# Performance work log

Hardware: AMD Instinct MI355X
Metric: run time of the kernel (lower is better)

## Reference

```python
import jax, jax.numpy as jnp
import numpy as np

D_MODEL, D_STATE, D_CONV, EXPAND, MLP_EXPAND = 1024, 16, 4, 2, 2
D_INNER = EXPAND * D_MODEL          # 2048
DT_RANK = D_MODEL // 16             # 64
B, L = 2, 1024


def setup_inputs() -> dict:
    key = jax.random.key(0)
    ks = jax.random.split(key, 16)
    s = 0.02
    inp = {
        "x": jax.random.normal(ks[0], (B, L, D_MODEL), jnp.float32),
        "ln1_w": jnp.ones((D_MODEL,), jnp.float32),
        "ln1_b": jnp.zeros((D_MODEL,), jnp.float32),
        "in_proj_w": jax.random.normal(ks[1], (2 * D_INNER, D_MODEL), jnp.float32) * s,
        "conv_w": jax.random.normal(ks[2], (D_INNER, 1, D_CONV), jnp.float32) * s,
        "conv_b": jnp.zeros((D_INNER,), jnp.float32),
        "x_proj_w": jax.random.normal(ks[3], (DT_RANK + 2 * D_STATE, D_INNER), jnp.float32) * s,
        "dt_proj_w": jax.random.normal(ks[4], (D_INNER, DT_RANK), jnp.float32) * s,
        "dt_proj_b": jax.random.uniform(ks[5], (D_INNER,), jnp.float32, -4.0, -2.0),
        "A_log": jnp.tile(jnp.log(jnp.arange(1, D_STATE + 1, dtype=jnp.float32))[None, :], (D_INNER, 1)),
        "D": jnp.ones((D_INNER,), jnp.float32),
        "out_proj_w": jax.random.normal(ks[6], (D_MODEL, D_INNER), jnp.float32) * s,
        "ln2_w": jnp.ones((D_MODEL,), jnp.float32),
        "ln2_b": jnp.zeros((D_MODEL,), jnp.float32),
        "mlp_w1": jax.random.normal(ks[7], (MLP_EXPAND * D_MODEL, D_MODEL), jnp.float32) * s,
        "mlp_b1": jnp.zeros((MLP_EXPAND * D_MODEL,), jnp.float32),
        "mlp_w2": jax.random.normal(ks[8], (D_MODEL, MLP_EXPAND * D_MODEL), jnp.float32) * s,
        "mlp_b2": jnp.zeros((D_MODEL,), jnp.float32),
    }
    return inp


def _layernorm(x, w, b, eps=1e-5):
    mu = jnp.mean(x, -1, keepdims=True)
    var = jnp.var(x, -1, keepdims=True)
    return (x - mu) * jax.lax.rsqrt(var + eps) * w + b


def _mamba(x, in_proj_w, conv_w, conv_b, x_proj_w, dt_proj_w, dt_proj_b, A_log, D, out_proj_w):
    # x: (B, L, d_model)
    xz = jnp.einsum('bld,ed->ble', x, in_proj_w)          # (B, L, 2*d_inner)
    u, z = jnp.split(xz, 2, axis=-1)                      # each (B, L, d_inner)
    # depthwise causal conv over time
    u_c = jnp.transpose(u, (0, 2, 1))                     # (B, d_inner, L)
    u_c = jax.lax.conv_general_dilated(
        u_c, conv_w, window_strides=(1,), padding=[(D_CONV - 1, 0)],
        dimension_numbers=('NCH', 'OIH', 'NCH'), feature_group_count=D_INNER)
    u = jax.nn.silu(jnp.transpose(u_c, (0, 2, 1)) + conv_b)  # (B, L, d_inner)

    dbc = jnp.einsum('bld,ed->ble', u, x_proj_w)          # (B, L, dt_rank+2*d_state)
    dt, Bm, Cm = jnp.split(dbc, [DT_RANK, DT_RANK + D_STATE], axis=-1)
    delta = jax.nn.softplus(jnp.einsum('blr,dr->bld', dt, dt_proj_w) + dt_proj_b)  # (B, L, d_inner)

    A = -jnp.exp(A_log)                                   # (d_inner, d_state)
    deltaA = jnp.exp(delta[..., None] * A)                # (B, L, d_inner, d_state)
    deltaBu = delta[..., None] * Bm[:, :, None, :] * u[..., None]

    def step(h, inp):
        dA, dBu, Ct = inp
        h = dA * h + dBu                                  # (B, d_inner, d_state)
        y = jnp.einsum('bdn,bn->bd', h, Ct)
        return h, y

    h0 = jnp.zeros((x.shape[0], D_INNER, D_STATE), x.dtype)
    xs = (jnp.moveaxis(deltaA, 1, 0), jnp.moveaxis(deltaBu, 1, 0), jnp.moveaxis(Cm, 1, 0))
    _, ys = jax.lax.scan(step, h0, xs)                    # (L, B, d_inner)
    y = jnp.moveaxis(ys, 0, 1) + u * D                    # (B, L, d_inner)
    y = y * jax.nn.silu(z)
    return jnp.einsum('ble,de->bld', y, out_proj_w)


def reference(x, ln1_w, ln1_b, in_proj_w, conv_w, conv_b, x_proj_w, dt_proj_w, dt_proj_b,
              A_log, D, out_proj_w, ln2_w, ln2_b, mlp_w1, mlp_b1, mlp_w2, mlp_b2):
    h = x + _mamba(_layernorm(x, ln1_w, ln1_b), in_proj_w, conv_w, conv_b,
                   x_proj_w, dt_proj_w, dt_proj_b, A_log, D, out_proj_w)
    y = _layernorm(h, ln2_w, ln2_b)
    y = jax.nn.gelu(jnp.einsum('bld,ed->ble', y, mlp_w1) + mlp_b1, approximate=False)
    y = jnp.einsum('ble,de->bld', y, mlp_w2) + mlp_b2
    return h + y
```

## Files before the change

kernel.cpp:

```cpp
#include <hip/hip_runtime.h>
#include <hip/hip_bf16.h>
#include <math.h>

typedef __hip_bfloat16 bf16;
typedef __attribute__((ext_vector_type(8))) short bf16x8;
typedef __attribute__((ext_vector_type(4))) float f32x4;

__device__ __forceinline__ float b2f(bf16 x) { return __bfloat162float(x); }
__device__ __forceinline__ float us2f(unsigned short u) {
    return __uint_as_float(((unsigned int)u) << 16);
}
__device__ __forceinline__ unsigned short f2us(float f) {
    bf16 t = __float2bfloat16(f);
    return *reinterpret_cast<unsigned short*>(&t);
}
__device__ __forceinline__ float scrub(float v) {
    return (v == v && fabsf(v) < 3.0e38f) ? v : 0.f;
}
__device__ __forceinline__ float to_float(float x) { return x; }
__device__ __forceinline__ float to_float(bf16 x) { return __bfloat162float(x); }
__device__ __forceinline__ void store_out(float* p, float v) { *p = v; }
__device__ __forceinline__ void store_out(bf16* p, float v) { *p = __float2bfloat16(v); }

__device__ __forceinline__ void cp16(const void* g, void* l) {
    __builtin_amdgcn_global_load_lds(
        (const __attribute__((address_space(1))) unsigned int*)g,
        (__attribute__((address_space(3))) unsigned int*)l, 16, 0, 0);
}

struct Ptrs { const void* p[18]; };

__constant__ __device__ const long TOFF[19] = {
    0,         2097152,  2098176,  2099200,  6293504,  6301696,  6303744,
    6500352,   6631424,  6633472,  6666240,  6668288,  8765440,  8766464,
    8767488,   10864640, 10866688, 12963840, 12964864};

__global__ __launch_bounds__(256) void convert_kernel(
    Ptrs ptrs, unsigned short* __restrict__ dst)
{
    const long g = (long)blockIdx.x * 256 + threadIdx.x;
    if (g >= 1620608) return;
    const long e0 = g * 8;
    int t = 0;
    #pragma unroll
    for (int i = 1; i < 18; ++i) t += (e0 >= TOFF[i]) ? 1 : 0;
    const long local = e0 - TOFF[t];
    const float4* ps = (const float4*)((const float*)ptrs.p[t] + local);
    const float4 a = ps[0], b = ps[1];
    ushort4 o0, o1;
    o0.x = f2us(a.x); o0.y = f2us(a.y); o0.z = f2us(a.z); o0.w = f2us(a.w);
    o1.x = f2us(b.x); o1.y = f2us(b.y); o1.z = f2us(b.z); o1.w = f2us(b.w);
    *(ushort4*)(dst + e0)     = o0;
    *(ushort4*)(dst + e0 + 4) = o1;
}

template <typename TIN>
__global__ __launch_bounds__(256) void ln_kernel(
    const TIN* __restrict__ in, const bf16* __restrict__ gw,
    const bf16* __restrict__ gb, bf16* __restrict__ out)
{
    const int row = blockIdx.x;
    const int tid = threadIdx.x;
    float v[4];
    if constexpr (sizeof(TIN) == 2) {
        ushort4 raw = ((const ushort4*)((const unsigned short*)in + (long)row * 1024))[tid];
        v[0] = us2f(raw.x); v[1] = us2f(raw.y); v[2] = us2f(raw.z); v[3] = us2f(raw.w);
    } else {
        float4 raw = ((const float4*)((const float*)in + (long)row * 1024))[tid];
        v[0] = raw.x; v[1] = raw.y; v[2] = raw.z; v[3] = raw.w;
    }
    float s  = v[0] + v[1] + v[2] + v[3];
    float s2 = v[0]*v[0] + v[1]*v[1] + v[2]*v[2] + v[3]*v[3];
    #pragma unroll
    for (int o = 32; o > 0; o >>= 1) {
        s  += __shfl_xor(s, o);
        s2 += __shfl_xor(s2, o);
    }
    __shared__ float red[8];
    if ((tid & 63) == 0) { red[tid >> 6] = s; red[4 + (tid >> 6)] = s2; }
    __syncthreads();
    s  = red[0] + red[1] + red[2] + red[3];
    s2 = red[4] + red[5] + red[6] + red[7];
    const float mu  = s * (1.f / 1024.f);
    const float var = fmaxf(s2 * (1.f / 1024.f) - mu * mu, 0.f);
    const float rs  = rsqrtf(var + 1e-5f);
    const int c0 = tid * 4;
    ushort4 o;
    o.x = f2us((v[0] - mu) * rs * b2f(gw[c0 + 0]) + b2f(gb[c0 + 0]));
    o.y = f2us((v[1] - mu) * rs * b2f(gw[c0 + 1]) + b2f(gb[c0 + 1]));
    o.z = f2us((v[2] - mu) * rs * b2f(gw[c0 + 2]) + b2f(gb[c0 + 2]));
    o.w = f2us((v[3] - mu) * rs * b2f(gw[c0 + 3]) + b2f(gb[c0 + 3]));
    ((ushort4*)((unsigned short*)out + (long)row * 1024))[tid] = o;
}

template <int BM, int BN, int ACT, bool NG, typename TOUT, typename TRES>
__global__ __launch_bounds__(256) void gemm_as(
    const bf16* __restrict__ A, int lda,
    const bf16* __restrict__ Bw, int ldb,
    TOUT* __restrict__ C, int ldc,
    const bf16* __restrict__ bias,
    const TRES* __restrict__ res,
    int M, int N, int K)
{
    constexpr int AI = BM / 32;
    constexpr int BJ = BN / 32;
    __shared__ __align__(16) short As[BM * 64];
    __shared__ __align__(16) short Bs[BN * 64];
    const int tid  = threadIdx.x;
    const int lane = tid & 63;
    const int wv   = tid >> 6;
    const int m0 = blockIdx.y * BM;
    const int n0 = blockIdx.x * BN;
    const int wm = (wv >> 1) * (BM / 2);
    const int wn = (wv & 1) * (BN / 2);
    const int lr = lane & 15;
    const int lq = lane >> 4;
    const int grow = lane >> 3;
    const int gcol = (lane & 7) * 8;

    if (NG) {
        const int z0 = (N - n0) * 64;
        uint4 z; z.x = z.y = z.z = z.w = 0;
        for (int s = z0 + tid * 8; s < BN * 64; s += 2048)
            *(uint4*)&Bs[s] = z;
    }

    f32x4 acc[AI][BJ] = {};

    for (int k0 = 0; k0 < K; k0 += 64) {
        #pragma unroll
        for (int g = 0; g < BM / 32; ++g) {
            const int gg = g * 4 + wv;
            cp16(A + (long)(m0 + gg * 8 + grow) * lda + k0 + gcol, &As[gg * 512]);
        }
        #pragma unroll
        for (int g = 0; g < BN / 32; ++g) {
            const int gg = g * 4 + wv;
            if (!NG || n0 + gg * 8 < N)
                cp16(Bw + (long)(n0 + gg * 8 + grow) * ldb + k0 + gcol, &Bs[gg * 512]);
        }
        __syncthreads();

        #pragma unroll
        for (int kk = 0; kk < 2; ++kk) {
            bf16x8 af[AI], bfr[BJ];
            #pragma unroll
            for (int i = 0; i < AI; ++i)
                af[i] = *(const bf16x8*)&As[(wm + i * 16 + lr) * 64 + kk * 32 + lq * 8];
            #pragma unroll
            for (int j = 0; j < BJ; ++j)
                bfr[j] = *(const bf16x8*)&Bs[(wn + j * 16 + lr) * 64 + kk * 32 + lq * 8];
            #pragma unroll
            for (int i = 0; i < AI; ++i)
                #pragma unroll
                for (int j = 0; j < BJ; ++j)
                    acc[i][j] = __builtin_amdgcn_mfma_f32_16x16x32_bf16(
                        af[i], bfr[j], acc[i][j], 0, 0, 0);
        }
        __syncthreads();
    }

    #pragma unroll
    for (int j = 0; j < BJ; ++j) {
        const int col = n0 + wn + j * 16 + lr;
        if (col >= N) continue;
        const float bv = bias ? b2f(bias[col]) : 0.f;
        #pragma unroll
        for (int i = 0; i < AI; ++i) {
            const int r0 = m0 + wm + i * 16 + lq * 4;
            #pragma unroll
            for (int r = 0; r < 4; ++r) {
                const long row = r0 + r;
                float v = acc[i][j][r] + bv;
                if (ACT == 1) v = 0.5f * v * (1.f + erff(v * 0.70710678118f));
                if (ACT == 2) v = (v > 20.f) ? v : log1pf(__expf(v));
                if (res) v += to_float(res[row * (long)ldc + col]);
                store_out(&C[row * (long)ldc + col], scrub(v));
            }
        }
    }
}

__global__ __launch_bounds__(256) void conv_silu_kernel(
    const bf16* __restrict__ xz, const bf16* __restrict__ cw,
    const bf16* __restrict__ cb, bf16* __restrict__ uc)
{
    const int gid = blockIdx.x * 256 + threadIdx.x;
    const int d   = gid & 2047;
    const int row = gid >> 11;
    const int t   = row & 1023;
    float acc = b2f(cb[d]);
    #pragma unroll
    for (int j = 0; j < 4; ++j) {
        const int tt = t - 3 + j;
        if (tt >= 0)
            acc += b2f(cw[d * 4 + j]) * b2f(xz[(long)(row - 3 + j) * 4096 + d]);
    }
    const float sg = 1.f / (1.f + __expf(-acc));
    uc[gid] = __float2bfloat16(acc * sg);
}

__global__ __launch_bounds__(256) void scan_kernel(
    const bf16* __restrict__ delta,
    const bf16* __restrict__ uc,
    const bf16* __restrict__ dbc,
    const bf16* __restrict__ xz,
    const float* __restrict__ A_log,
    const float* __restrict__ Dp,
    bf16* __restrict__ y)
{
    const int b   = blockIdx.y;
    const int d0  = blockIdx.x * 16;
    const int tid = threadIdx.x;
    const int n   = tid & 15;
    const int dl  = tid >> 4;
    const int d   = d0 + dl;

    __shared__ float2 sDU[64][16];
    __shared__ float2 sBC[64][16];
    __shared__ float  sZ [64][16];
    __shared__ float  sP [64][16][20];

    const float An = -expf(A_log[d * 16 + n]);
    const float Dd = Dp[d];
    float h = 0.f;
    const long rowbase = (long)b * 1024;

    const int dl3 = tid & 15;
    const int t3  = tid >> 4;

    float rDT[4], rUV[4], rB[4], rC[4], rZ[4];
    auto load_chunk = [&](int t0c) {
        #pragma unroll
        for (int k = 0; k < 4; ++k) {
            const int i  = k * 256 + tid;
            const int tt = i >> 4, dd = i & 15;
            const long r = rowbase + t0c + tt;
            rDT[k] = b2f(delta[r * 2048 + d0 + dd]);
            rUV[k] = b2f(uc   [r * 2048 + d0 + dd]);
            rB[k]  = b2f(dbc  [r * 96 + 64 + dd]);
            rC[k]  = b2f(dbc  [r * 96 + 80 + dd]);
            rZ[k]  = b2f(xz   [r * 4096 + 2048 + d0 + dd]);
        }
    };
    auto store_chunk = [&]() {
        #pragma unroll
        for (int k = 0; k < 4; ++k) {
            const int i  = k * 256 + tid;
            const int tt = i >> 4, dd = i & 15;
            sDU[tt][dd] = float2{rDT[k], rUV[k]};
            sBC[tt][dd] = float2{rB[k], rC[k]};
            const float zz = rZ[k];
            sZ[tt][dd] = zz / (1.f + __expf(-zz));
        }
    };

    load_chunk(0);
    for (int t0 = 0; t0 < 1024; t0 += 64) {
        store_chunk();
        __syncthreads();
        if (t0 + 64 < 1024) load_chunk(t0 + 64);

        {
            float2 dua[8], bca[8], dub[8], bcb[8];
            #pragma unroll
            for (int t = 0; t < 8; ++t) { dua[t] = sDU[t][dl]; bca[t] = sBC[t][n]; }
            #pragma unroll
            for (int tb = 0; tb < 64; tb += 8) {
                if (tb < 56) {
                    #pragma unroll
                    for (int t = 0; t < 8; ++t) {
                        dub[t] = sDU[tb + 8 + t][dl];
                        bcb[t] = sBC[tb + 8 + t][n];
                    }
                }
                #pragma unroll
                for (int t = 0; t < 8; ++t) {
                    const float a = __expf(dua[t].x * An);
                    h = a * h + (dua[t].x * dua[t].y) * bca[t].x;
                    float p = h * bca[t].y;
                    if (n == 0) p += dua[t].y * Dd;
                    sP[tb + t][dl][n] = p;
                }
                #pragma unroll
                for (int t = 0; t < 8; ++t) { dua[t] = dub[t]; bca[t] = bcb[t]; }
            }
        }
        __syncthreads();

        #pragma unroll
        for (int k = 0; k < 4; ++k) {
            const int t = t3 + k * 16;
            const float4* pp = (const float4*)&sP[t][dl3][0];
            const float4 p0 = pp[0], p1 = pp[1], p2 = pp[2], p3 = pp[3];
            const float s = ((p0.x + p0.y) + (p0.z + p0.w))
                          + ((p1.x + p1.y) + (p1.z + p1.w))
                          + ((p2.x + p2.y) + (p2.z + p2.w))
                          + ((p3.x + p3.y) + (p3.z + p3.w));
            const float yv = s * sZ[t][dl3];
            y[(rowbase + t0 + t) * 2048 + d0 + dl3] = __float2bfloat16(yv);
        }
        __syncthreads();
    }
}

extern "C" void kernel_launch(void* const* d_in, const int* in_sizes, int n_in,
                              void* d_out, int out_size, void* d_ws, size_t ws_size,
                              hipStream_t stream)
{
    char* ws = (char*)d_ws;
    const size_t MiB = 1048576;

    bf16*  xn  = (bf16*)(ws);
    bf16*  xz  = (bf16*)(ws +  4 * MiB);
    bf16*  uc  = (bf16*)(ws + 20 * MiB);
    bf16*  dbc = (bf16*)(ws + 28 * MiB);
    bf16*  dlb = (bf16*)(ws + 28 * MiB + 524288);
    bf16*  yb  = dlb;
    float* hb  = (float*)(ws);
    bf16*  hn  = (bf16*)(ws +  8 * MiB);
    bf16*  gb  = (bf16*)(ws + 12 * MiB);
    unsigned short* cvt = (unsigned short*)(ws + 37 * MiB);

    const float* xf     = (const float*)d_in[0];
    const float* A_logf = (const float*)d_in[9];
    const float* Dpf    = (const float*)d_in[10];

    const bf16* ln1_w      = (const bf16*)(cvt + 2097152);
    const bf16* ln1_b      = (const bf16*)(cvt + 2098176);
    const bf16* in_proj_w  = (const bf16*)(cvt + 2099200);
    const bf16* conv_w     = (const bf16*)(cvt + 6293504);
    const bf16* conv_b     = (const bf16*)(cvt + 6301696);
    const bf16* x_proj_w   = (const bf16*)(cvt + 6303744);
    const bf16* dt_proj_w  = (const bf16*)(cvt + 6500352);
    const bf16* dt_proj_b  = (const bf16*)(cvt + 6631424);
    const bf16* out_proj_w = (const bf16*)(cvt + 6668288);
    const bf16* ln2_w      = (const bf16*)(cvt + 8765440);
    const bf16* ln2_b      = (const bf16*)(cvt + 8766464);
    const bf16* mlp_w1     = (const bf16*)(cvt + 8767488);
    const bf16* mlp_b1     = (const bf16*)(cvt + 10864640);
    const bf16* mlp_w2     = (const bf16*)(cvt + 10866688);
    const bf16* mlp_b2     = (const bf16*)(cvt + 12963840);

    Ptrs ptrs;
    for (int i = 0; i < 18; ++i) ptrs.p[i] = d_in[i];
    convert_kernel<<<6332, 256, 0, stream>>>(ptrs, cvt);

    ln_kernel<float><<<2048, 256, 0, stream>>>(xf, ln1_w, ln1_b, xn);
    gemm_as<128, 128, 0, false, bf16, bf16><<<dim3(32, 16), 256, 0, stream>>>(
        xn, 1024, in_proj_w, 1024, xz, 4096, nullptr, (const bf16*)nullptr, 2048, 4096, 1024);
    conv_silu_kernel<<<16384, 256, 0, stream>>>(xz, conv_w, conv_b, uc);
    gemm_as<64, 64, 0, true, bf16, bf16><<<dim3(2, 32), 256, 0, stream>>>(
        uc, 2048, x_proj_w, 2048, dbc, 96, nullptr, (const bf16*)nullptr, 2048, 96, 2048);
    gemm_as<64, 64, 2, false, bf16, bf16><<<dim3(32, 32), 256, 0, stream>>>(
        dbc, 96, dt_proj_w, 64, dlb, 2048, dt_proj_b, (const bf16*)nullptr, 2048, 2048, 64);
    scan_kernel<<<dim3(128, 2), 256, 0, stream>>>(dlb, uc, dbc, xz, A_logf, Dpf, yb);
    gemm_as<64, 64, 0, false, float, float><<<dim3(16, 32), 256, 0, stream>>>(
        yb, 2048, out_proj_w, 2048, hb, 1024, nullptr, xf, 2048, 1024, 2048);
    ln_kernel<float><<<2048, 256, 0, stream>>>(hb, ln2_w, ln2_b, hn);
    gemm_as<64, 64, 1, false, bf16, bf16><<<dim3(32, 32), 256, 0, stream>>>(
        hn, 1024, mlp_w1, 1024, gb, 2048, mlp_b1, (const bf16*)nullptr, 2048, 2048, 1024);
    gemm_as<64, 64, 0, false, float, float><<<dim3(16, 32), 256, 0, stream>>>(
        gb, 2048, mlp_w2, 2048, (float*)d_out, 1024, mlp_b2, hb, 2048, 1024, 2048);
}
```

Baseline: 362.8 us.

## Split selective scan into chunked local scan, carry combine, and fix-up passes

Replaces the single sequential scan over 1024 timesteps (256 blocks) with a three-phase chunked scan. The sequence is split into 8 segments of 128 steps, each scanned locally from a zero state (2048 blocks), and the cumulative delta sums are stored in bf16. A small combine kernel then propagates the carried states across segments, and a fix-up kernel adds the C·exp(A·P)·h_in correction to each output. SiLU(z) is moved into the conv kernel, which now writes u and silu(z) interleaved. The goal is more parallelism on the latency-bound scan, at the cost of extra passes, more memory traffic, and bf16 rounding of the cumulative delta inside the exponent.

```diff
diff --git a/kernel.cpp b/kernel.cpp
--- a/kernel.cpp
+++ b/kernel.cpp
@@ -183,7 +183,7 @@
 
 __global__ __launch_bounds__(256) void conv_silu_kernel(
     const bf16* __restrict__ xz, const bf16* __restrict__ cw,
-    const bf16* __restrict__ cb, bf16* __restrict__ uc)
+    const bf16* __restrict__ cb, bf16* __restrict__ ucz)
 {
     const int gid = blockIdx.x * 256 + threadIdx.x;
     const int d   = gid & 2047;
@@ -196,111 +196,186 @@
         if (tt >= 0)
             acc += b2f(cw[d * 4 + j]) * b2f(xz[(long)(row - 3 + j) * 4096 + d]);
     }
-    const float sg = 1.f / (1.f + __expf(-acc));
-    uc[gid] = __float2bfloat16(acc * sg);
-}
-
-__global__ __launch_bounds__(256) void scan_kernel(
+    ucz[(long)row * 4096 + d] = __float2bfloat16(acc / (1.f + __expf(-acc)));
+    const float zz = b2f(xz[(long)row * 4096 + 2048 + d]);
+    ucz[(long)row * 4096 + 2048 + d] = __float2bfloat16(zz / (1.f + __expf(-zz)));
+}
+
+__global__ __launch_bounds__(256) void scan_local_kernel(
     const bf16* __restrict__ delta,
-    const bf16* __restrict__ uc,
+    const bf16* __restrict__ ucz,
     const bf16* __restrict__ dbc,
-    const bf16* __restrict__ xz,
     const float* __restrict__ A_log,
     const float* __restrict__ Dp,
-    bf16* __restrict__ y)
-{
+    bf16* __restrict__ y_local,
+    bf16* __restrict__ Pbuf,
+    float* __restrict__ h_out)
+{
+    const int d0  = blockIdx.x * 16;
     const int b   = blockIdx.y;
-    const int d0  = blockIdx.x * 16;
+    const int sg  = blockIdx.z;
     const int tid = threadIdx.x;
     const int n   = tid & 15;
     const int dl  = tid >> 4;
     const int d   = d0 + dl;
 
-    __shared__ float2 sDU[64][16];
-    __shared__ float2 sBC[64][16];
-    __shared__ float  sZ [64][16];
-    __shared__ float  sP [64][16][20];
+    __shared__ float2         sDU[32][16];
+    __shared__ float2         sBC[32][16];
+    __shared__ float          sZ [32][16];
+    __shared__ unsigned short sPc[32][16];
+    __shared__ unsigned short sY [32][16];
+    __shared__ float          sP [32][16][20];
 
     const float An = -expf(A_log[d * 16 + n]);
     const float Dd = Dp[d];
-    float h = 0.f;
-    const long rowbase = (long)b * 1024;
-
-    const int dl3 = tid & 15;
-    const int t3  = tid >> 4;
-
-    float rDT[4], rUV[4], rB[4], rC[4], rZ[4];
+    float h = 0.f, Pc = 0.f;
+    const long rowbase = (long)b * 1024 + sg * 128;
+
+    const int wv  = tid >> 6;
+    const int pdl = 4 * wv + ((tid & 63) >> 4);
+    const int ptq = tid & 15;
+
+    float rDT[2], rUV[2], rB[2], rC[2], rZ[2];
     auto load_chunk = [&](int t0c) {
         #pragma unroll
-        for (int k = 0; k < 4; ++k) {
+        for (int k = 0; k < 2; ++k) {
             const int i  = k * 256 + tid;
             const int tt = i >> 4, dd = i & 15;
             const long r = rowbase + t0c + tt;
             rDT[k] = b2f(delta[r * 2048 + d0 + dd]);
-            rUV[k] = b2f(uc   [r * 2048 + d0 + dd]);
+            rUV[k] = b2f(ucz  [r * 4096 + d0 + dd]);
             rB[k]  = b2f(dbc  [r * 96 + 64 + dd]);
             rC[k]  = b2f(dbc  [r * 96 + 80 + dd]);
-            rZ[k]  = b2f(xz   [r * 4096 + 2048 + d0 + dd]);
+            rZ[k]  = b2f(ucz  [r * 4096 + 2048 + d0 + dd]);
         }
     };
     auto store_chunk = [&]() {
         #pragma unroll
-        for (int k = 0; k < 4; ++k) {
+        for (int k = 0; k < 2; ++k) {
             const int i  = k * 256 + tid;
             const int tt = i >> 4, dd = i & 15;
             sDU[tt][dd] = float2{rDT[k], rUV[k]};
             sBC[tt][dd] = float2{rB[k], rC[k]};
-            const float zz = rZ[k];
-            sZ[tt][dd] = zz / (1.f + __expf(-zz));
+            sZ[tt][dd]  = rZ[k];
         }
     };
 
     load_chunk(0);
-    for (int t0 = 0; t0 < 1024; t0 += 64) {
+    for (int t0 = 0; t0 < 128; t0 += 32) {
         store_chunk();
         __syncthreads();
-        if (t0 + 64 < 1024) load_chunk(t0 + 64);
-
-        {
-            float2 dua[8], bca[8], dub[8], bcb[8];
-            #pragma unroll
-            for (int t = 0; t < 8; ++t) { dua[t] = sDU[t][dl]; bca[t] = sBC[t][n]; }
-            #pragma unroll
-            for (int tb = 0; tb < 64; tb += 8) {
-                if (tb < 56) {
-                    #pragma unroll
-                    for (int t = 0; t < 8; ++t) {
-                        dub[t] = sDU[tb + 8 + t][dl];
-                        bcb[t] = sBC[tb + 8 + t][n];
-                    }
-                }
-                #pragma unroll
-                for (int t = 0; t < 8; ++t) {
-                    const float a = __expf(dua[t].x * An);
-                    h = a * h + (dua[t].x * dua[t].y) * bca[t].x;
-                    float p = h * bca[t].y;
-                    if (n == 0) p += dua[t].y * Dd;
-                    sP[tb + t][dl][n] = p;
-                }
-                #pragma unroll
-                for (int t = 0; t < 8; ++t) { dua[t] = dub[t]; bca[t] = bcb[t]; }
-            }
-        }
-        __syncthreads();
-
-        #pragma unroll
-        for (int k = 0; k < 4; ++k) {
-            const int t = t3 + k * 16;
-            const float4* pp = (const float4*)&sP[t][dl3][0];
+        if (t0 + 32 < 128) load_chunk(t0 + 32);
+
+        #pragma unroll 4
+        for (int t = 0; t < 32; ++t) {
+            const float2 du = sDU[t][dl];
+            const float2 bc = sBC[t][n];
+            Pc += du.x;
+            const float a = __expf(du.x * An);
+            h = a * h + (du.x * du.y) * bc.x;
+            float p = h * bc.y;
+            if (n == 0) { p += du.y * Dd; sPc[t][dl] = f2us(Pc); }
+            sP[t][dl][n] = p;
+        }
+
+        #pragma unroll
+        for (int k = 0; k < 2; ++k) {
+            const int t = ptq + k * 16;
+            const float4* pp = (const float4*)&sP[t][pdl][0];
             const float4 p0 = pp[0], p1 = pp[1], p2 = pp[2], p3 = pp[3];
             const float s = ((p0.x + p0.y) + (p0.z + p0.w))
                           + ((p1.x + p1.y) + (p1.z + p1.w))
                           + ((p2.x + p2.y) + (p2.z + p2.w))
                           + ((p3.x + p3.y) + (p3.z + p3.w));
-            const float yv = s * sZ[t][dl3];
-            y[(rowbase + t0 + t) * 2048 + d0 + dl3] = __float2bfloat16(yv);
+            sY[t][pdl] = f2us(s * sZ[t][pdl]);
         }
         __syncthreads();
+
+        #pragma unroll
+        for (int k = 0; k < 2; ++k) {
+            const int i  = k * 256 + tid;
+            const int tt = i >> 4, dd = i & 15;
+            const long r = rowbase + t0 + tt;
+            ((unsigned short*)y_local)[r * 2048 + d0 + dd] = sY[tt][dd];
+            ((unsigned short*)Pbuf)  [r * 2048 + d0 + dd] = sPc[tt][dd];
+        }
+        __syncthreads();
+    }
+
+    h_out[((long)(b * 8 + sg) * 2048 + d) * 16 + n] = h;
+}
+
+__global__ __launch_bounds__(256) void scan_combine_kernel(
+    const bf16*  __restrict__ Pbuf,
+    const float* __restrict__ A_log,
+    const float* __restrict__ h_out,
+    float* __restrict__ h_in)
+{
+    const int gid = blockIdx.x * 256 + threadIdx.x;
+    const int b  = gid >> 15;
+    const int dn = gid & 32767;
+    const int d  = dn >> 4;
+    const float An = -expf(A_log[dn]);
+    float hin = 0.f;
+    h_in[(long)(b * 8) * 32768 + dn] = 0.f;
+    for (int s = 0; s < 7; ++s) {
+        const float Pend = us2f(((const unsigned short*)Pbuf)
+                                [((long)b * 1024 + s * 128 + 127) * 2048 + d]);
+        const float hout = h_out[(long)(b * 8 + s) * 32768 + dn];
+        hin = hout + __expf(An * Pend) * hin;
+        h_in[(long)(b * 8 + s + 1) * 32768 + dn] = hin;
+    }
+}
+
+__global__ __launch_bounds__(256) void scan_fix_kernel(
+    bf16* __restrict__ y,
+    const bf16* __restrict__ Pbuf,
+    const bf16* __restrict__ dbc,
+    const bf16* __restrict__ ucz,
+    const float* __restrict__ A_log,
+    const float* __restrict__ h_in)
+{
+    const int d0  = blockIdx.x * 16;
+    const int b   = blockIdx.y;
+    const int sg  = blockIdx.z;
+    const int tid = threadIdx.x;
+    const long rowb = (long)b * 1024 + sg * 128;
+
+    __shared__ float sH [16][16];
+    __shared__ float sAn[16][16];
+    __shared__ float sCc[128][16];
+
+    sH [tid >> 4][tid & 15] = h_in[(long)(b * 8 + sg) * 32768 + d0 * 16 + tid];
+    sAn[tid >> 4][tid & 15] = -expf(A_log[d0 * 16 + tid]);
+    for (int i = tid; i < 2048; i += 256)
+        sCc[i >> 4][i & 15] = b2f(dbc[(rowb + (i >> 4)) * 96 + 80 + (i & 15)]);
+    __syncthreads();
+
+    const int dd = tid & 15;
+    float4 An4[4], H4[4];
+    #pragma unroll
+    for (int j = 0; j < 4; ++j) {
+        An4[j] = *(const float4*)&sAn[dd][j * 4];
+        H4[j]  = *(const float4*)&sH [dd][j * 4];
+    }
+
+    #pragma unroll
+    for (int k = 0; k < 8; ++k) {
+        const int t = k * 16 + (tid >> 4);
+        const long row = rowb + t;
+        const float P = us2f(((const unsigned short*)Pbuf)[row * 2048 + d0 + dd]);
+        float corr = 0.f;
+        #pragma unroll
+        for (int j = 0; j < 4; ++j) {
+            const float4 C4 = *(const float4*)&sCc[t][j * 4];
+            corr += C4.x * __expf(An4[j].x * P) * H4[j].x;
+            corr += C4.y * __expf(An4[j].y * P) * H4[j].y;
+            corr += C4.z * __expf(An4[j].z * P) * H4[j].z;
+            corr += C4.w * __expf(An4[j].w * P) * H4[j].w;
+        }
+        const float slz = b2f(ucz[row * 4096 + 2048 + d0 + dd]);
+        const float yl  = b2f(y[row * 2048 + d0 + dd]);
+        y[row * 2048 + d0 + dd] = __float2bfloat16(yl + slz * corr);
     }
 }
 
@@ -310,16 +385,19 @@
 {
     char* ws = (char*)d_ws;
     const size_t MiB = 1048576;
-
-    bf16*  xn  = (bf16*)(ws);
-    bf16*  xz  = (bf16*)(ws +  4 * MiB);
-    bf16*  uc  = (bf16*)(ws + 20 * MiB);
-    bf16*  dbc = (bf16*)(ws + 28 * MiB);
-    bf16*  dlb = (bf16*)(ws + 28 * MiB + 524288);
-    bf16*  yb  = dlb;
-    float* hb  = (float*)(ws);
-    bf16*  hn  = (bf16*)(ws +  8 * MiB);
-    bf16*  gb  = (bf16*)(ws + 12 * MiB);
+    const size_t HMiB = 524288;
+
+    bf16*  ucz  = (bf16*)(ws);
+    bf16*  dbc  = (bf16*)(ws + 16 * MiB);
+    bf16*  xn   = (bf16*)(ws + 16 * MiB + HMiB);
+    bf16*  dlb  = (bf16*)(ws + 16 * MiB + HMiB);
+    bf16*  xz   = (bf16*)(ws + 20 * MiB + HMiB);
+    bf16*  Pbuf = (bf16*)(ws + 24 * MiB + HMiB);
+    float* hout = (float*)(ws + 32 * MiB + HMiB);
+    float* hin  = (float*)(ws + 34 * MiB + HMiB);
+    float* hb   = (float*)(ws);
+    bf16*  hn   = (bf16*)(ws +  8 * MiB);
+    bf16*  gb   = (bf16*)(ws + 24 * MiB + HMiB);
     unsigned short* cvt = (unsigned short*)(ws + 37 * MiB);
 
     const float* xf     = (const float*)d_in[0];
@@ -349,14 +427,18 @@
     ln_kernel<float><<<2048, 256, 0, stream>>>(xf, ln1_w, ln1_b, xn);
     gemm_as<128, 128, 0, false, bf16, bf16><<<dim3(32, 16), 256, 0, stream>>>(
         xn, 1024, in_proj_w, 1024, xz, 4096, nullptr, (const bf16*)nullptr, 2048, 4096, 1024);
-    conv_silu_kernel<<<16384, 256, 0, stream>>>(xz, conv_w, conv_b, uc);
+    conv_silu_kernel<<<16384, 256, 0, stream>>>(xz, conv_w, conv_b, ucz);
     gemm_as<64, 64, 0, true, bf16, bf16><<<dim3(2, 32), 256, 0, stream>>>(
-        uc, 2048, x_proj_w, 2048, dbc, 96, nullptr, (const bf16*)nullptr, 2048, 96, 2048);
+        ucz, 4096, x_proj_w, 2048, dbc, 96, nullptr, (const bf16*)nullptr, 2048, 96, 2048);
     gemm_as<64, 64, 2, false, bf16, bf16><<<dim3(32, 32), 256, 0, stream>>>(
         dbc, 96, dt_proj_w, 64, dlb, 2048, dt_proj_b, (const bf16*)nullptr, 2048, 2048, 64);
-    scan_kernel<<<dim3(128, 2), 256, 0, stream>>>(dlb, uc, dbc, xz, A_logf, Dpf, yb);
+    scan_local_kernel<<<dim3(128, 2, 8), 256, 0, stream>>>(
+        dlb, ucz, dbc, A_logf, Dpf, dlb, Pbuf, hout);
+    scan_combine_kernel<<<256, 256, 0, stream>>>(Pbuf, A_logf, hout, hin);
+    scan_fix_kernel<<<dim3(128, 2, 8), 256, 0, stream>>>(
+        dlb, Pbuf, dbc, ucz, A_logf, hin);
     gemm_as<64, 64, 0, false, float, float><<<dim3(16, 32), 256, 0, stream>>>(
-        yb, 2048, out_proj_w, 2048, hb, 1024, nullptr, xf, 2048, 1024, 2048);
+        dlb, 2048, out_proj_w, 2048, hb, 1024, nullptr, xf, 2048, 1024, 2048);
     ln_kernel<float><<<2048, 256, 0, stream>>>(hb, ln2_w, ln2_b, hn);
     gemm_as<64, 64, 1, false, bf16, bf16><<<dim3(32, 32), 256, 0, stream>>>(
         hn, 1024, mlp_w1, 1024, gb, 2048, mlp_b1, (const bf16*)nullptr, 2048, 2048, 1024);
```

Measured after the change: 398.8 us. 9.9% more time.
